# Kernel optimization log

Hardware: AMD Instinct MI355X
Metric: run time of the kernel (lower is better)

## Reference

```python
import jax, jax.numpy as jnp
import numpy as np

GAMMA = 0.001

def softor(x, axis, gamma=GAMMA):
    # gamma * logsumexp(x/gamma); renormalize by global max if it exceeds 1 (NSFR convention)
    s = gamma * jax.nn.logsumexp(x / gamma, axis=axis)
    m = jnp.max(s)
    return jnp.where(m > 1.0, s / m, s)

def softand(x, axis, gamma=GAMMA):
    # soft conjunction: -gamma * logsumexp(-x/gamma) (soft-min), same renormalization
    s = -gamma * jax.nn.logsumexp(-x / gamma, axis=axis)
    m = jnp.max(s)
    return jnp.where(m > 1.0, s / m, s)

def clause_fn(x, I_c):
    # x: (B, G) valuations; I_c: (G, S, L) atom indices for one clause.
    # torch.gather(V_tild, 1, I_tild)[b,g,s,l] == x[b, I_c[g,s,l]] -> plain take.
    g = jnp.take(x, I_c, axis=1)        # (B, G, S, L)
    p = softand(g, axis=3)              # (B, G, S): conjunction over body literals
    return softor(p, axis=2)            # (B, G): disjunction over substitutions

def setup_inputs() -> dict:
    key = jax.random.key(0)
    k1, k2 = jax.random.split(key)
    C, B, G, S, L = 16, 64, 2048, 8, 4
    x = jax.random.uniform(k1, (B, G), dtype=jnp.float32)
    I = jax.random.randint(k2, (C, G, S, L), 0, G, dtype=jnp.int32)
    return {"x": x, "I": I, "infer_step": 3}

def reference(x, I, infer_step):
    C = I.shape[0]
    R = jnp.broadcast_to(x[None], (C,) + x.shape)   # (C, B, G)
    def step(R, _):
        # r(R): one ClauseFunction per clause, vmapped over the clause axis
        r_R = jax.vmap(clause_fn)(R, I)             # (C, B, G)
        # softor([R, r_R], dim=2): stack along a new axis at position 2, reduce it
        R_new = softor(jnp.stack([R, r_R], axis=2), axis=2)
        return R_new, None
    R, _ = jax.lax.scan(step, R, None, length=infer_step)
    return R
```

## Files before the change

### kernel.cpp

```cpp
#include <hip/hip_runtime.h>


namespace {
constexpr int C = 16, B = 64, G = 2048, S = 8, L = 4;
constexpr int STEPS = 3;
}

__device__ __forceinline__ float4 f4min(float4 a, float4 b) {
    return make_float4(fminf(a.x,b.x), fminf(a.y,b.y), fminf(a.z,b.z), fminf(a.w,b.w));
}
__device__ __forceinline__ float4 f4max(float4 a, float4 b) {
    return make_float4(fmaxf(a.x,b.x), fmaxf(a.y,b.y), fmaxf(a.z,b.z), fmaxf(a.w,b.w));
}

__global__ __launch_bounds__(1024) void k_all(const float* __restrict__ x,
                                              const int* __restrict__ I,
                                              float* __restrict__ out) {
    __shared__ float4 lds4[G];

    const int tid = threadIdx.x;
    const int bq = blockIdx.x & 15, c = blockIdx.x >> 4;
    const int b0 = bq * 4;
    const int ga = tid, gb = tid + 1024;

    const int4* Ipa = (const int4*)(I + (size_t)(c * G + ga) * (S * L));
    const int4* Ipb = (const int4*)(I + (size_t)(c * G + gb) * (S * L));
    int4 ixa[S], ixb[S];
#pragma unroll
    for (int s = 0; s < S; ++s) { ixa[s] = Ipa[s]; ixb[s] = Ipb[s]; }

    float2 pr[4];
#pragma unroll
    for (int j = 0; j < 4; ++j)
        pr[j] = ((const float2*)(x + (size_t)(b0 + j) * G))[tid];
    lds4[2 * tid]     = make_float4(pr[0].x, pr[1].x, pr[2].x, pr[3].x);
    lds4[2 * tid + 1] = make_float4(pr[0].y, pr[1].y, pr[2].y, pr[3].y);
    __syncthreads();

#pragma unroll
    for (int step = 0; step < STEPS; ++step) {
        float4 qa = make_float4(-3.0e38f, -3.0e38f, -3.0e38f, -3.0e38f);
        float4 qb = qa;
#pragma unroll
        for (int s = 0; s < S; ++s) {
            int4 iv = ixa[s];
            qa = f4max(qa, f4min(f4min(lds4[iv.x], lds4[iv.y]),
                                 f4min(lds4[iv.z], lds4[iv.w])));
            iv = ixb[s];
            qb = f4max(qb, f4min(f4min(lds4[iv.x], lds4[iv.y]),
                                 f4min(lds4[iv.z], lds4[iv.w])));
        }
        const float4 sa = f4max(lds4[ga], qa);
        const float4 sb = f4max(lds4[gb], qb);

        if (step < STEPS - 1) {
            __syncthreads();
            lds4[ga] = sa;
            lds4[gb] = sb;
            __syncthreads();
        } else {
            out[(size_t)(c * B + b0 + 0) * G + ga] = sa.x;
            out[(size_t)(c * B + b0 + 1) * G + ga] = sa.y;
            out[(size_t)(c * B + b0 + 2) * G + ga] = sa.z;
            out[(size_t)(c * B + b0 + 3) * G + ga] = sa.w;
            out[(size_t)(c * B + b0 + 0) * G + gb] = sb.x;
            out[(size_t)(c * B + b0 + 1) * G + gb] = sb.y;
            out[(size_t)(c * B + b0 + 2) * G + gb] = sb.z;
            out[(size_t)(c * B + b0 + 3) * G + gb] = sb.w;
        }
    }
}

extern "C" void kernel_launch(void* const* d_in, const int* in_sizes, int n_in,
                              void* d_out, int out_size, void* d_ws, size_t ws_size,
                              hipStream_t stream) {
    const float* x = (const float*)d_in[0];
    const int*   I = (const int*)d_in[1];
    float* out = (float*)d_out;

    k_all<<<C * 16, 1024, 0, stream>>>(x, I, out);
}
```

Measured before the change: 97.88 us.

## Store LDS valuations as packed fp16 and double-buffer steps to drop a barrier

Converts the shared valuation table from float4 to packed half4, halving LDS bytes per gather and using packed fp16 min/max. Adds ping-pong LDS buffers and keeps each thread's own values in registers, removing one barrier per inference step. Output precision drops to fp16 rounding of the valuations, which may affect tolerance.

```diff
diff --git a/kernel.cpp b/kernel.cpp
--- a/kernel.cpp
+++ b/kernel.cpp
@@ -6,17 +6,15 @@
 constexpr int STEPS = 3;
 }
 
-__device__ __forceinline__ float4 f4min(float4 a, float4 b) {
-    return make_float4(fminf(a.x,b.x), fminf(a.y,b.y), fminf(a.z,b.z), fminf(a.w,b.w));
-}
-__device__ __forceinline__ float4 f4max(float4 a, float4 b) {
-    return make_float4(fmaxf(a.x,b.x), fmaxf(a.y,b.y), fmaxf(a.z,b.z), fmaxf(a.w,b.w));
-}
+typedef _Float16 h4 __attribute__((ext_vector_type(4)));
+
+__device__ __forceinline__ h4 h4min(h4 a, h4 b) { return __builtin_elementwise_min(a, b); }
+__device__ __forceinline__ h4 h4max(h4 a, h4 b) { return __builtin_elementwise_max(a, b); }
 
 __global__ __launch_bounds__(1024) void k_all(const float* __restrict__ x,
                                               const int* __restrict__ I,
                                               float* __restrict__ out) {
-    __shared__ float4 lds4[G];
+    __shared__ h4 buf[2][G];
 
     const int tid = threadIdx.x;
     const int bq = blockIdx.x & 15, c = blockIdx.x >> 4;
@@ -33,40 +31,51 @@
 #pragma unroll
     for (int j = 0; j < 4; ++j)
         pr[j] = ((const float2*)(x + (size_t)(b0 + j) * G))[tid];
-    lds4[2 * tid]     = make_float4(pr[0].x, pr[1].x, pr[2].x, pr[3].x);
-    lds4[2 * tid + 1] = make_float4(pr[0].y, pr[1].y, pr[2].y, pr[3].y);
+    {
+        h4 t0, t1;
+        t0[0] = (_Float16)pr[0].x; t0[1] = (_Float16)pr[1].x;
+        t0[2] = (_Float16)pr[2].x; t0[3] = (_Float16)pr[3].x;
+        t1[0] = (_Float16)pr[0].y; t1[1] = (_Float16)pr[1].y;
+        t1[2] = (_Float16)pr[2].y; t1[3] = (_Float16)pr[3].y;
+        buf[0][2 * tid]     = t0;
+        buf[0][2 * tid + 1] = t1;
+    }
     __syncthreads();
+    h4 cura = buf[0][ga];
+    h4 curb = buf[0][gb];
 
 #pragma unroll
     for (int step = 0; step < STEPS; ++step) {
-        float4 qa = make_float4(-3.0e38f, -3.0e38f, -3.0e38f, -3.0e38f);
-        float4 qb = qa;
+        const h4* rd = buf[step & 1];
+        h4* wr = buf[(step & 1) ^ 1];
+
+        int4 iv = ixa[0];
+        h4 qa = h4min(h4min(rd[iv.x], rd[iv.y]), h4min(rd[iv.z], rd[iv.w]));
+        iv = ixb[0];
+        h4 qb = h4min(h4min(rd[iv.x], rd[iv.y]), h4min(rd[iv.z], rd[iv.w]));
 #pragma unroll
-        for (int s = 0; s < S; ++s) {
-            int4 iv = ixa[s];
-            qa = f4max(qa, f4min(f4min(lds4[iv.x], lds4[iv.y]),
-                                 f4min(lds4[iv.z], lds4[iv.w])));
+        for (int s = 1; s < S; ++s) {
+            iv = ixa[s];
+            qa = h4max(qa, h4min(h4min(rd[iv.x], rd[iv.y]), h4min(rd[iv.z], rd[iv.w])));
             iv = ixb[s];
-            qb = f4max(qb, f4min(f4min(lds4[iv.x], lds4[iv.y]),
-                                 f4min(lds4[iv.z], lds4[iv.w])));
+            qb = h4max(qb, h4min(h4min(rd[iv.x], rd[iv.y]), h4min(rd[iv.z], rd[iv.w])));
         }
-        const float4 sa = f4max(lds4[ga], qa);
-        const float4 sb = f4max(lds4[gb], qb);
+        cura = h4max(cura, qa);
+        curb = h4max(curb, qb);
 
         if (step < STEPS - 1) {
-            __syncthreads();
-            lds4[ga] = sa;
-            lds4[gb] = sb;
+            wr[ga] = cura;
+            wr[gb] = curb;
             __syncthreads();
         } else {
-            out[(size_t)(c * B + b0 + 0) * G + ga] = sa.x;
-            out[(size_t)(c * B + b0 + 1) * G + ga] = sa.y;
-            out[(size_t)(c * B + b0 + 2) * G + ga] = sa.z;
-            out[(size_t)(c * B + b0 + 3) * G + ga] = sa.w;
-            out[(size_t)(c * B + b0 + 0) * G + gb] = sb.x;
-            out[(size_t)(c * B + b0 + 1) * G + gb] = sb.y;
-            out[(size_t)(c * B + b0 + 2) * G + gb] = sb.z;
-            out[(size_t)(c * B + b0 + 3) * G + gb] = sb.w;
+            out[(size_t)(c * B + b0 + 0) * G + ga] = (float)cura[0];
+            out[(size_t)(c * B + b0 + 1) * G + ga] = (float)cura[1];
+            out[(size_t)(c * B + b0 + 2) * G + ga] = (float)cura[2];
+            out[(size_t)(c * B + b0 + 3) * G + ga] = (float)cura[3];
+            out[(size_t)(c * B + b0 + 0) * G + gb] = (float)curb[0];
+            out[(size_t)(c * B + b0 + 1) * G + gb] = (float)curb[1];
+            out[(size_t)(c * B + b0 + 2) * G + gb] = (float)curb[2];
+            out[(size_t)(c * B + b0 + 3) * G + gb] = (float)curb[3];
         }
     }
 }
```

New measurement: 84.16 us. 14.0% less time.
